# Performance work log

Hardware: AMD Instinct MI355X
Metric: run time of the kernel (lower is better)

Reference implementation:

```python
import jax, jax.numpy as jnp
import numpy as np

VIEW_NUM = 360
CHAN_NUM = 512
BATCH = 2
IMG = 512


def setup_inputs() -> dict:
    key = jax.random.key(0)
    x = jax.random.normal(key, (BATCH, 1, IMG, IMG), dtype=jnp.float32)
    return {"x": x}


def _bilinear_sample_zeros(img, ix, iy):
    """Bilinear sample img (B,1,H,W) at pixel coords ix, iy (H,W), zeros padding.
    Matches F.grid_sample(mode='bilinear', padding_mode='zeros', align_corners=False)."""
    H, W = img.shape[-2], img.shape[-1]
    x0 = jnp.floor(ix)
    y0 = jnp.floor(iy)
    x1 = x0 + 1.0
    y1 = y0 + 1.0
    wx1 = ix - x0
    wx0 = 1.0 - wx1
    wy1 = iy - y0
    wy0 = 1.0 - wy1

    def gather(yy, xx):
        valid = (xx >= 0) & (xx <= W - 1) & (yy >= 0) & (yy <= H - 1)
        xi = jnp.clip(xx, 0, W - 1).astype(jnp.int32)
        yi = jnp.clip(yy, 0, H - 1).astype(jnp.int32)
        # fancy-index over spatial dims -> (B,1,H,W)
        return img[:, :, yi, xi] * valid.astype(img.dtype)

    return (gather(y0, x0) * (wy0 * wx0)
            + gather(y0, x1) * (wy0 * wx1)
            + gather(y1, x0) * (wy1 * wx0)
            + gather(y1, x1) * (wy1 * wx1))


def _fp(x):
    B, C, H, W = x.shape
    # affine_grid base coords, align_corners=False: (2i+1)/N - 1
    bx = (2.0 * jnp.arange(W, dtype=x.dtype) + 1.0) / W - 1.0
    by = (2.0 * jnp.arange(H, dtype=x.dtype) + 1.0) / H - 1.0
    X = bx[None, :]  # (1,W)
    Y = by[:, None]  # (H,1)
    i = jnp.arange(VIEW_NUM, dtype=x.dtype)
    angles = -jnp.pi * (i + 1.0) / VIEW_NUM - jnp.pi
    cosv = jnp.cos(angles)
    sinv = jnp.sin(angles)

    def per_view(carry, cs):
        c, s = cs
        # theta = [[c,-s,0],[s,c,0]]; grid = base @ theta^T
        gx = c * X - s * Y  # (H,W) normalized sample x
        gy = s * X + c * Y  # (H,W) normalized sample y
        # unnormalize (align_corners=False)
        ix = ((gx + 1.0) * W - 1.0) * 0.5
        iy = ((gy + 1.0) * H - 1.0) * 0.5
        samp = _bilinear_sample_zeros(x, ix, iy)  # (B,1,H,W)
        return carry, jnp.sum(samp, axis=2)  # sum over height -> (B,1,W)

    _, cols = jax.lax.scan(per_view, 0, (cosv, sinv))  # (V,B,1,W)
    sino = jnp.transpose(cols, (1, 2, 3, 0)) * 0.5  # (B,1,chanNum,viewNum)
    return sino


def reference(x):
    return _fp(x)
```

## Files before the change

kernel.cpp:

```cpp
#include <hip/hip_runtime.h>

typedef __fp16 h2 __attribute__((ext_vector_type(2)));

constexpr int VIEWS = 360;
constexpr int IMGSZ = 512;
constexpr int WCHUNK = 64;
constexpr int KH = 64;
constexpr int MAXNY = 94;
constexpr int LDSDW = 9800;
constexpr int PW = 712;
constexpr int PH = 704;
constexpr int PAD = 96;

#define ASYNC_CP16(SRC, DST)                                              \
    __builtin_amdgcn_global_load_lds(                                     \
        (const __attribute__((address_space(1))) unsigned*)(SRC),         \
        (__attribute__((address_space(3))) unsigned*)(DST), 16, 0, 0)

__global__ __launch_bounds__(256) void pad_kernel(const float* __restrict__ x,
                                                  unsigned* __restrict__ padq) {
    constexpr int PW4 = PW / 4;
    constexpr int total = PH * PW4;
    int idx = blockIdx.x * 256 + threadIdx.x;
    if (idx >= total) return;
    int py = idx / PW4;
    int px4 = idx - py * PW4;
    int gx = px4 * 4 - PAD;
    int gy = py - PAD;
    const float* img0 = x;
    const float* img1 = x + (size_t)IMGSZ * IMGSZ;
    float4 a = make_float4(0.f, 0.f, 0.f, 0.f);
    float4 bq = a;
    if ((unsigned)gy < (unsigned)IMGSZ && (unsigned)gx < (unsigned)IMGSZ) {
        size_t off = (size_t)gy * IMGSZ + gx;
        a  = *(const float4*)(img0 + off);
        bq = *(const float4*)(img1 + off);
    }
    uint4 d;
    d.x = __builtin_bit_cast(unsigned, __builtin_amdgcn_cvt_pkrtz(a.x, bq.x));
    d.y = __builtin_bit_cast(unsigned, __builtin_amdgcn_cvt_pkrtz(a.y, bq.y));
    d.z = __builtin_bit_cast(unsigned, __builtin_amdgcn_cvt_pkrtz(a.z, bq.z));
    d.w = __builtin_bit_cast(unsigned, __builtin_amdgcn_cvt_pkrtz(a.w, bq.w));
    *(uint4*)&padq[(size_t)idx * 4] = d;
}

__global__ __launch_bounds__(256) void fp_kernel(const unsigned* __restrict__ padq,
                                                 float* __restrict__ out) {
    __shared__ __align__(16) unsigned tileU[LDSDW];

    int blk = blockIdx.x;
    int wc = blk & 7;
    int v = blk >> 3;

    int tid = threadIdx.x;
    int lane = tid & 63;
    int g = tid >> 6;
    int w = wc * WCHUNK + lane;

    double ang = -3.14159265358979323846 * (double)(v + 1) / (double)VIEWS
                 - 3.14159265358979323846;
    float c = (float)cos(ang);
    float s = (float)sin(ang);

    int NYbb = min((int)(63.0f * (fabsf(s) + fabsf(c))) + 6, MAXNY);
    int bestj = 0, bestsc = 1000;
#pragma unroll
    for (int j = 0; j < 4; ++j) {
        int Pj = 100 + 4 * j;
        if (Pj * NYbb > LDSDW) break;
        float t = fmaf((float)Pj, s, c);
        float rm = rintf(t);
        float dl = fabsf(t - rm);
        int m = (int)rm;
        int am = m & 31;
        int sc;
        if (am & 1)              sc = 0;
        else if (m == 0)         sc = 1;
        else if (dl >= 0.22f)    sc = 2;
        else if ((am & 3) == 2)  sc = 2;
        else if ((am & 7) == 4)  sc = 4;
        else if ((am & 15) == 8) sc = 6;
        else if (am == 16)       sc = 8;
        else                     sc = 10;
        if (sc < bestsc) { bestsc = sc; bestj = j; }
    }
    int P = 100 + 4 * bestj;
    int NXW = P >> 2;
    unsigned mgc = (bestj == 0) ? 10486u : (bestj == 1) ? 10083u
                 : (bestj == 2) ? 9710u : 9363u;
    int stepRow = PW - P;

    float xw = (float)w + 0.5f - 256.0f;
    float cxw = fmaf(c, xw, 255.5f);
    float sxw = fmaf(s, xw, 255.5f);

    float lo = -1e30f, hi = 1e30f;
    {
        float coef = -s, base = cxw;
        if (fabsf(coef) > 1e-6f) {
            float a = (-1.0f - base) / coef;
            float bq = (512.0f - base) / coef;
            lo = fmaxf(lo, fminf(a, bq));
            hi = fminf(hi, fmaxf(a, bq));
        } else if (!(base > -1.0f && base < 512.0f)) {
            lo = 1e30f; hi = -1e30f;
        }
    }
    {
        float coef = c, base = sxw;
        if (fabsf(coef) > 1e-6f) {
            float a = (-1.0f - base) / coef;
            float bq = (512.0f - base) / coef;
            lo = fmaxf(lo, fminf(a, bq));
            hi = fminf(hi, fmaxf(a, bq));
        } else if (!(base > -1.0f && base < 512.0f)) {
            lo = 1e30f; hi = -1e30f;
        }
    }
    float h0f = fminf(fmaxf(floorf(lo + 255.5f) - 1.0f, 0.0f), 512.0f);
    float h1f = fminf(fmaxf(ceilf(hi + 255.5f) + 1.0f, -1.0f), 511.0f);
    int h0 = (int)h0f;
    int h1 = (int)h1f;

    int bh0 = h0, bh1 = h1;
    #pragma unroll
    for (int m = 1; m < 64; m <<= 1) {
        bh0 = min(bh0, __shfl_xor(bh0, m, 64));
        bh1 = max(bh1, __shfl_xor(bh1, m, 64));
    }

    float xa = (float)(wc * WCHUNK) + 0.5f - 256.0f;
    float xb = xa + 63.0f;

    float acc0 = 0.0f, acc1 = 0.0f;
    float step4x = -4.0f * s;
    float step4y = 4.0f * c;

    for (int hc = bh0; hc <= bh1; hc += KH) {
        int hend = min(hc + KH - 1, bh1);

        float ha = (float)hc - 255.5f;
        float hb = (float)hend - 255.5f;
        float ix00 = c * xa - s * ha, ix01 = c * xa - s * hb;
        float ix10 = c * xb - s * ha, ix11 = c * xb - s * hb;
        float iy00 = s * xa + c * ha, iy01 = s * xa + c * hb;
        float iy10 = s * xb + c * ha, iy11 = s * xb + c * hb;
        float ixmn = fminf(fminf(ix00, ix01), fminf(ix10, ix11)) + 255.5f;
        float iymn = fminf(fminf(iy00, iy01), fminf(iy10, iy11)) + 255.5f;
        float iymx = fmaxf(fmaxf(iy00, iy01), fmaxf(iy10, iy11)) + 255.5f;
        int x_lo = (int)floorf(ixmn) - 1;
        int x_lo4 = x_lo & ~3;
        int y_lo = (int)floorf(iymn) - 1;
        int NY = min((int)floorf(iymx) + 3 - y_lo, MAXNY);
        int total4 = NY * NXW;
        int nit = (total4 + 255) >> 8;

        __syncthreads();

        {
            const unsigned* pb = padq + (y_lo + PAD) * PW + (x_lo4 + PAD);
            for (int k = 0; k < nit; ++k) {
                int i = (k << 8) + tid;
                if (((k << 8) + (g << 6) + 63) < total4) {
                    unsigned ry = ((unsigned)i * mgc) >> 18;
                    ASYNC_CP16(pb + 4 * i + stepRow * (int)ry, &tileU[i << 2]);
                } else if (i < total4) {
                    unsigned ry = ((unsigned)i * mgc) >> 18;
                    uint4 val = *(const uint4*)(pb + 4 * i + stepRow * (int)ry);
                    *(uint4*)&tileU[i << 2] = val;
                }
            }
        }
        asm volatile("s_waitcnt vmcnt(0)" ::: "memory");
        __syncthreads();

        float hh0 = (float)(hc + g) - 255.5f;
        float ixr = fmaf(-s, hh0, cxw) - (float)x_lo4;
        float iyr = fmaf(c, hh0, sxw) - (float)y_lo;
        h2 accp0 = (h2)0.0f;
        h2 accp1 = (h2)0.0f;
        int parity = 0;
        #pragma unroll 8
        for (int h = hc + g; h <= hend; h += 4) {
            float fx = floorf(ixr);
            float fy = floorf(iyr);
            int lx = (int)fx;
            int ly = (int)fy;
            float wx1 = ixr - fx;
            float wy1 = iyr - fy;
            h2 wxs = __builtin_amdgcn_cvt_pkrtz(wx1, wx1);
            h2 wys = __builtin_amdgcn_cvt_pkrtz(wy1, wy1);
            const unsigned* p = tileU + (ly * P + lx);
            const unsigned* q = p + P;
            h2 t00 = __builtin_bit_cast(h2, p[0]);
            h2 t01 = __builtin_bit_cast(h2, p[1]);
            h2 t10 = __builtin_bit_cast(h2, q[0]);
            h2 t11 = __builtin_bit_cast(h2, q[1]);
            h2 r0 = t00 + (t01 - t00) * wxs;
            h2 r1 = t10 + (t11 - t10) * wxs;
            h2 contrib = r0 + (r1 - r0) * wys;
            if (parity) accp1 += contrib; else accp0 += contrib;
            parity ^= 1;
            ixr += step4x;
            iyr += step4y;
        }
        acc0 += (float)accp0.x + (float)accp1.x;
        acc1 += (float)accp0.y + (float)accp1.y;
    }

    __syncthreads();
    tileU[(g << 6) + lane] = __float_as_uint(acc0);
    tileU[256 + (g << 6) + lane] = __float_as_uint(acc1);
    __syncthreads();
    if (g == 0) {
        float r0 = __uint_as_float(tileU[lane]) + __uint_as_float(tileU[64 + lane]) +
                   __uint_as_float(tileU[128 + lane]) + __uint_as_float(tileU[192 + lane]);
        float r1 = __uint_as_float(tileU[256 + lane]) + __uint_as_float(tileU[320 + lane]) +
                   __uint_as_float(tileU[384 + lane]) + __uint_as_float(tileU[448 + lane]);
        size_t o = (size_t)w * VIEWS + v;
        out[o] = r0 * 0.5f;
        out[(size_t)IMGSZ * VIEWS + o] = r1 * 0.5f;
    }
}

extern "C" void kernel_launch(void* const* d_in, const int* in_sizes, int n_in,
                              void* d_out, int out_size, void* d_ws, size_t ws_size,
                              hipStream_t stream) {
    const float* x = (const float*)d_in[0];
    float* out = (float*)d_out;
    unsigned* padq = (unsigned*)d_ws;

    constexpr int padTotal = PH * (PW / 4);
    pad_kernel<<<(padTotal + 255) / 256, 256, 0, stream>>>(x, padq);

    int nblocks = VIEWS * (IMGSZ / WCHUNK);
    fp_kernel<<<nblocks, 256, 0, stream>>>(padq, out);
}
```

Before: 153.6 us.

## Add transposed lane-over-height sampling mode chosen by LDS bank-conflict score

Adds a second per-view work mapping in which lanes walk different image rows (h) while each wave loops over 16 output columns, accumulating per-column fp16 partials that are reduced with wave shuffles. A continuous bank-conflict score function now picks both the LDS tile pitch (including a new 96/108 option) and which mapping to use, so views whose original access pattern causes LDS bank conflicts can use the other stride. Per-wave height bounds are shared through LDS to set the block range, and waves skip chunks outside their own range. The cost is more register pressure from 16 accumulators, 16 shuffle reductions per block, and extra control flow and divergence between views.

```diff
diff --git a/kernel.cpp b/kernel.cpp
--- a/kernel.cpp
+++ b/kernel.cpp
@@ -44,6 +44,40 @@
     *(uint4*)&padq[(size_t)idx * 4] = d;
 }
 
+__device__ __forceinline__ float conflict_score(float d) {
+    float ad = fabsf(d);
+    float m = ad - 32.0f * floorf(ad * 0.03125f);
+    float r = rintf(m);
+    float eta = fabsf(m - r);
+    int ri = ((int)r) & 31;
+    float base;
+    if (ri & 1)       base = 0.0f;
+    else if (ri == 0) base = (ad < 0.5f) ? 0.6f : 8.0f;
+    else if (ri & 2)  base = 1.0f;
+    else if (ri & 4)  base = 2.2f;
+    else if (ri & 8)  base = 4.0f;
+    else              base = 6.0f;
+    return base * fmaxf(0.0f, 1.0f - 4.0f * eta);
+}
+
+__device__ __forceinline__ void cons_bounds(float coef, float ba, float bb,
+                                            float& lo, float& hi) {
+    if (fabsf(coef) > 1e-6f) {
+        float la = (-1.0f - ba) / coef, ha = (512.0f - ba) / coef;
+        float lb = (-1.0f - bb) / coef, hb = (512.0f - bb) / coef;
+        lo = fminf(fminf(la, ha), fminf(lb, hb));
+        hi = fmaxf(fmaxf(la, ha), fmaxf(lb, hb));
+    } else {
+        bool ina = (ba > -1.0f) && (ba < 512.0f);
+        bool inb = (bb > -1.0f) && (bb < 512.0f);
+        if (!ina && !inb && ((ba <= -1.0f) == (bb <= -1.0f))) {
+            lo = 1e30f; hi = -1e30f;
+        } else {
+            lo = -1e30f; hi = 1e30f;
+        }
+    }
+}
+
 __global__ __launch_bounds__(256) void fp_kernel(const unsigned* __restrict__ padq,
                                                  float* __restrict__ out) {
     __shared__ __align__(16) unsigned tileU[LDSDW];
@@ -62,77 +96,105 @@
     float c = (float)cos(ang);
     float s = (float)sin(ang);
 
-    int NYbb = min((int)(63.0f * (fabsf(s) + fabsf(c))) + 6, MAXNY);
-    int bestj = 0, bestsc = 1000;
-#pragma unroll
-    for (int j = 0; j < 4; ++j) {
-        int Pj = 100 + 4 * j;
-        if (Pj * NYbb > LDSDW) break;
-        float t = fmaf((float)Pj, s, c);
-        float rm = rintf(t);
-        float dl = fabsf(t - rm);
-        int m = (int)rm;
-        int am = m & 31;
-        int sc;
-        if (am & 1)              sc = 0;
-        else if (m == 0)         sc = 1;
-        else if (dl >= 0.22f)    sc = 2;
-        else if ((am & 3) == 2)  sc = 2;
-        else if ((am & 7) == 4)  sc = 4;
-        else if ((am & 15) == 8) sc = 6;
-        else if (am == 16)       sc = 8;
-        else                     sc = 10;
-        if (sc < bestsc) { bestsc = sc; bestj = j; }
-    }
-    int P = 100 + 4 * bestj;
+    float as_ = fabsf(s), ac_ = fabsf(c);
+    int sxi = (int)(63.0f * (as_ + ac_)) + 6;
+    int NYbb = min(sxi, MAXNY);
+    int bestP = 100, bestMode = 0;
+    float bestSc = conflict_score(c + 100.0f * s);
+    {
+        float sB0 = conflict_score(c * 100.0f - s) + 0.25f;
+        if (sB0 < bestSc) { bestSc = sB0; bestMode = 1; }
+    }
+    #pragma unroll
+    for (int pi = 0; pi < 5; ++pi) {
+        int P = 96 + 4 * pi;
+        if (P == 100) continue;
+        if (P < sxi + 2) continue;
+        if (P * NYbb > LDSDW) continue;
+        float fP = (float)P;
+        float sA = conflict_score(c + fP * s) + 0.02f * (float)pi;
+        float sB = conflict_score(c * fP - s) + 0.02f * (float)pi + 0.25f;
+        if (sA < bestSc) { bestSc = sA; bestP = P; bestMode = 0; }
+        if (sB < bestSc) { bestSc = sB; bestP = P; bestMode = 1; }
+    }
+    int P = bestP;
+    int mode = bestMode;
     int NXW = P >> 2;
-    unsigned mgc = (bestj == 0) ? 10486u : (bestj == 1) ? 10083u
-                 : (bestj == 2) ? 9710u : 9363u;
+    unsigned mgc = (262144u + (unsigned)NXW - 1u) / (unsigned)NXW;
     int stepRow = PW - P;
+    int NYcap = min(MAXNY, LDSDW / P);
 
     float xw = (float)w + 0.5f - 256.0f;
     float cxw = fmaf(c, xw, 255.5f);
     float sxw = fmaf(s, xw, 255.5f);
 
-    float lo = -1e30f, hi = 1e30f;
-    {
-        float coef = -s, base = cxw;
-        if (fabsf(coef) > 1e-6f) {
-            float a = (-1.0f - base) / coef;
-            float bq = (512.0f - base) / coef;
-            lo = fmaxf(lo, fminf(a, bq));
-            hi = fminf(hi, fmaxf(a, bq));
-        } else if (!(base > -1.0f && base < 512.0f)) {
-            lo = 1e30f; hi = -1e30f;
-        }
-    }
-    {
-        float coef = c, base = sxw;
-        if (fabsf(coef) > 1e-6f) {
-            float a = (-1.0f - base) / coef;
-            float bq = (512.0f - base) / coef;
-            lo = fmaxf(lo, fminf(a, bq));
-            hi = fminf(hi, fmaxf(a, bq));
-        } else if (!(base > -1.0f && base < 512.0f)) {
-            lo = 1e30f; hi = -1e30f;
-        }
-    }
-    float h0f = fminf(fmaxf(floorf(lo + 255.5f) - 1.0f, 0.0f), 512.0f);
-    float h1f = fminf(fmaxf(ceilf(hi + 255.5f) + 1.0f, -1.0f), 511.0f);
-    int h0 = (int)h0f;
-    int h1 = (int)h1f;
-
-    int bh0 = h0, bh1 = h1;
-    #pragma unroll
-    for (int m = 1; m < 64; m <<= 1) {
-        bh0 = min(bh0, __shfl_xor(bh0, m, 64));
-        bh1 = max(bh1, __shfl_xor(bh1, m, 64));
-    }
-
     float xa = (float)(wc * WCHUNK) + 0.5f - 256.0f;
     float xb = xa + 63.0f;
 
+    int bh0, bh1;
+    int wh0 = 0, wh1 = -1;
+    if (mode == 0) {
+        float lo = -1e30f, hi = 1e30f;
+        {
+            float coef = -s, base = cxw;
+            if (fabsf(coef) > 1e-6f) {
+                float a = (-1.0f - base) / coef;
+                float bq = (512.0f - base) / coef;
+                lo = fmaxf(lo, fminf(a, bq));
+                hi = fminf(hi, fmaxf(a, bq));
+            } else if (!(base > -1.0f && base < 512.0f)) {
+                lo = 1e30f; hi = -1e30f;
+            }
+        }
+        {
+            float coef = c, base = sxw;
+            if (fabsf(coef) > 1e-6f) {
+                float a = (-1.0f - base) / coef;
+                float bq = (512.0f - base) / coef;
+                lo = fmaxf(lo, fminf(a, bq));
+                hi = fminf(hi, fmaxf(a, bq));
+            } else if (!(base > -1.0f && base < 512.0f)) {
+                lo = 1e30f; hi = -1e30f;
+            }
+        }
+        float h0f = fminf(fmaxf(floorf(lo + 255.5f) - 1.0f, 0.0f), 512.0f);
+        float h1f = fminf(fmaxf(ceilf(hi + 255.5f) + 1.0f, -1.0f), 511.0f);
+        int h0 = (int)h0f;
+        int h1 = (int)h1f;
+        bh0 = h0; bh1 = h1;
+        #pragma unroll
+        for (int m = 1; m < 64; m <<= 1) {
+            bh0 = min(bh0, __shfl_xor(bh0, m, 64));
+            bh1 = max(bh1, __shfl_xor(bh1, m, 64));
+        }
+    } else {
+        float xwa = (float)(wc * WCHUNK + (g << 4)) + 0.5f - 256.0f;
+        float xwb = xwa + 15.0f;
+        float lo1, hi1, lo2, hi2;
+        cons_bounds(-s, fmaf(c, xwa, 255.5f), fmaf(c, xwb, 255.5f), lo1, hi1);
+        cons_bounds(c,  fmaf(s, xwa, 255.5f), fmaf(s, xwb, 255.5f), lo2, hi2);
+        float wlo = fmaxf(lo1, lo2), whi = fminf(hi1, hi2);
+        wh0 = (int)fminf(fmaxf(floorf(wlo + 255.5f) - 1.0f, 0.0f), 512.0f);
+        wh1 = (int)fminf(fmaxf(ceilf(whi + 255.5f) + 1.0f, -1.0f), 511.0f);
+        if (lane == 0) {
+            tileU[(g << 1)] = (unsigned)(wh0 + 1024);
+            tileU[(g << 1) + 1] = (unsigned)(wh1 + 1024);
+        }
+        __syncthreads();
+        int b0 = 1 << 30, b1 = -(1 << 30);
+        #pragma unroll
+        for (int q2 = 0; q2 < 4; ++q2) {
+            b0 = min(b0, (int)tileU[(q2 << 1)] - 1024);
+            b1 = max(b1, (int)tileU[(q2 << 1) + 1] - 1024);
+        }
+        bh0 = b0; bh1 = b1;
+        __syncthreads();
+    }
+
     float acc0 = 0.0f, acc1 = 0.0f;
+    h2 accB[16];
+    #pragma unroll
+    for (int j = 0; j < 16; ++j) accB[j] = (h2)0.0f;
     float step4x = -4.0f * s;
     float step4y = 4.0f * c;
 
@@ -151,7 +213,7 @@
         int x_lo = (int)floorf(ixmn) - 1;
         int x_lo4 = x_lo & ~3;
         int y_lo = (int)floorf(iymn) - 1;
-        int NY = min((int)floorf(iymx) + 3 - y_lo, MAXNY);
+        int NY = min((int)floorf(iymx) + 3 - y_lo, NYcap);
         int total4 = NY * NXW;
         int nit = (total4 + 255) >> 8;
 
@@ -174,52 +236,106 @@
         asm volatile("s_waitcnt vmcnt(0)" ::: "memory");
         __syncthreads();
 
-        float hh0 = (float)(hc + g) - 255.5f;
-        float ixr = fmaf(-s, hh0, cxw) - (float)x_lo4;
-        float iyr = fmaf(c, hh0, sxw) - (float)y_lo;
-        h2 accp0 = (h2)0.0f;
-        h2 accp1 = (h2)0.0f;
-        int parity = 0;
-        #pragma unroll 8
-        for (int h = hc + g; h <= hend; h += 4) {
-            float fx = floorf(ixr);
-            float fy = floorf(iyr);
-            int lx = (int)fx;
-            int ly = (int)fy;
-            float wx1 = ixr - fx;
-            float wy1 = iyr - fy;
-            h2 wxs = __builtin_amdgcn_cvt_pkrtz(wx1, wx1);
-            h2 wys = __builtin_amdgcn_cvt_pkrtz(wy1, wy1);
-            const unsigned* p = tileU + (ly * P + lx);
-            const unsigned* q = p + P;
-            h2 t00 = __builtin_bit_cast(h2, p[0]);
-            h2 t01 = __builtin_bit_cast(h2, p[1]);
-            h2 t10 = __builtin_bit_cast(h2, q[0]);
-            h2 t11 = __builtin_bit_cast(h2, q[1]);
-            h2 r0 = t00 + (t01 - t00) * wxs;
-            h2 r1 = t10 + (t11 - t10) * wxs;
-            h2 contrib = r0 + (r1 - r0) * wys;
-            if (parity) accp1 += contrib; else accp0 += contrib;
-            parity ^= 1;
-            ixr += step4x;
-            iyr += step4y;
-        }
-        acc0 += (float)accp0.x + (float)accp1.x;
-        acc1 += (float)accp0.y + (float)accp1.y;
-    }
-
-    __syncthreads();
-    tileU[(g << 6) + lane] = __float_as_uint(acc0);
-    tileU[256 + (g << 6) + lane] = __float_as_uint(acc1);
-    __syncthreads();
-    if (g == 0) {
-        float r0 = __uint_as_float(tileU[lane]) + __uint_as_float(tileU[64 + lane]) +
-                   __uint_as_float(tileU[128 + lane]) + __uint_as_float(tileU[192 + lane]);
-        float r1 = __uint_as_float(tileU[256 + lane]) + __uint_as_float(tileU[320 + lane]) +
-                   __uint_as_float(tileU[384 + lane]) + __uint_as_float(tileU[448 + lane]);
-        size_t o = (size_t)w * VIEWS + v;
-        out[o] = r0 * 0.5f;
-        out[(size_t)IMGSZ * VIEWS + o] = r1 * 0.5f;
+        if (mode == 0) {
+            float hh0 = (float)(hc + g) - 255.5f;
+            float ixr = fmaf(-s, hh0, cxw) - (float)x_lo4;
+            float iyr = fmaf(c, hh0, sxw) - (float)y_lo;
+            h2 accp0 = (h2)0.0f;
+            h2 accp1 = (h2)0.0f;
+            int parity = 0;
+            #pragma unroll 8
+            for (int h = hc + g; h <= hend; h += 4) {
+                float fx = floorf(ixr);
+                float fy = floorf(iyr);
+                int lx = (int)fx;
+                int ly = (int)fy;
+                float wx1 = ixr - fx;
+                float wy1 = iyr - fy;
+                h2 wxs = __builtin_amdgcn_cvt_pkrtz(wx1, wx1);
+                h2 wys = __builtin_amdgcn_cvt_pkrtz(wy1, wy1);
+                const unsigned* p = tileU + (ly * P + lx);
+                const unsigned* q = p + P;
+                h2 t00 = __builtin_bit_cast(h2, p[0]);
+                h2 t01 = __builtin_bit_cast(h2, p[1]);
+                h2 t10 = __builtin_bit_cast(h2, q[0]);
+                h2 t11 = __builtin_bit_cast(h2, q[1]);
+                h2 r0 = t00 + (t01 - t00) * wxs;
+                h2 r1 = t10 + (t11 - t10) * wxs;
+                h2 contrib = r0 + (r1 - r0) * wys;
+                if (parity) accp1 += contrib; else accp0 += contrib;
+                parity ^= 1;
+                ixr += step4x;
+                iyr += step4y;
+            }
+            acc0 += (float)accp0.x + (float)accp1.x;
+            acc1 += (float)accp0.y + (float)accp1.y;
+        } else if (!(wh1 < hc || wh0 > hend)) {
+            bool vld = (hc + lane) <= hend;
+            float hlc = (float)min(hc + lane, hend) - 255.5f;
+            float SL = s * hlc;
+            float CL = c * hlc;
+            float xwj = (float)(wc * WCHUNK + (g << 4)) + 0.5f - 256.0f;
+            float U = fmaf(c, xwj, 255.5f) - (float)x_lo4;
+            float V = fmaf(s, xwj, 255.5f) - (float)y_lo;
+            #pragma unroll
+            for (int j = 0; j < 16; ++j) {
+                float ixr = U - SL;
+                float iyr = V + CL;
+                float fx = floorf(ixr);
+                float fy = floorf(iyr);
+                int lx = (int)fx;
+                int ly = (int)fy;
+                float wx1 = ixr - fx;
+                float wy1 = iyr - fy;
+                h2 wxs = __builtin_amdgcn_cvt_pkrtz(wx1, wx1);
+                h2 wys = __builtin_amdgcn_cvt_pkrtz(wy1, wy1);
+                const unsigned* p = tileU + (ly * P + lx);
+                const unsigned* q = p + P;
+                h2 t00 = __builtin_bit_cast(h2, p[0]);
+                h2 t01 = __builtin_bit_cast(h2, p[1]);
+                h2 t10 = __builtin_bit_cast(h2, q[0]);
+                h2 t11 = __builtin_bit_cast(h2, q[1]);
+                h2 r0 = t00 + (t01 - t00) * wxs;
+                h2 r1 = t10 + (t11 - t10) * wxs;
+                h2 contrib = r0 + (r1 - r0) * wys;
+                accB[j] += vld ? contrib : (h2)0.0f;
+                U += c;
+                V += s;
+            }
+        }
+    }
+
+    if (mode == 0) {
+        __syncthreads();
+        tileU[(g << 6) + lane] = __float_as_uint(acc0);
+        tileU[256 + (g << 6) + lane] = __float_as_uint(acc1);
+        __syncthreads();
+        if (g == 0) {
+            float r0 = __uint_as_float(tileU[lane]) + __uint_as_float(tileU[64 + lane]) +
+                       __uint_as_float(tileU[128 + lane]) + __uint_as_float(tileU[192 + lane]);
+            float r1 = __uint_as_float(tileU[256 + lane]) + __uint_as_float(tileU[320 + lane]) +
+                       __uint_as_float(tileU[384 + lane]) + __uint_as_float(tileU[448 + lane]);
+            size_t o = (size_t)w * VIEWS + v;
+            out[o] = r0 * 0.5f;
+            out[(size_t)IMGSZ * VIEWS + o] = r1 * 0.5f;
+        }
+    } else {
+        #pragma unroll
+        for (int j = 0; j < 16; ++j) {
+            float a0 = (float)accB[j].x;
+            float a1 = (float)accB[j].y;
+            #pragma unroll
+            for (int m = 1; m < 64; m <<= 1) {
+                a0 += __shfl_xor(a0, m, 64);
+                a1 += __shfl_xor(a1, m, 64);
+            }
+            if (lane == 0) {
+                int wj = wc * WCHUNK + (g << 4) + j;
+                size_t o = (size_t)wj * VIEWS + v;
+                out[o] = a0 * 0.5f;
+                out[(size_t)IMGSZ * VIEWS + o] = a1 * 0.5f;
+            }
+        }
     }
 }
 
```

Result: slower. 166.6 us (+8.5%).
